# Kernel optimization log

Measured on AMD Instinct MI355X. Metric: run time of the kernel, lower is better.

## Reference

```python
import jax, jax.numpy as jnp
import numpy as np

N, E, CIN, CHID, DIM, KS = 6000, 192000, 32, 64, 3, 5
K = KS ** DIM          # 125 total spline kernel weights
S = 2 ** DIM           # 8 nonzero linear B-spline basis products per edge


def spline_conv(x, edge_index, pseudo, W, root, bias):
    """SplineConv, degree-1 open B-spline, mean aggregation, root weight + bias.
    x: [N, Cin], edge_index: [2, E], pseudo: [E, DIM] in [0,1],
    W: [K, Cin, Cout], root: [Cin, Cout], bias: [Cout].
    """
    src, dst = edge_index[0], edge_index[1]
    cin = x.shape[1]
    # open spline: KS-1 intervals over [0,1]
    u = pseudo * (KS - 1)                               # [E, DIM]
    i0 = jnp.clip(jnp.floor(u), 0, KS - 2).astype(jnp.int32)
    frac = u - i0                                       # [E, DIM]
    bits = (jnp.arange(S)[:, None] >> jnp.arange(DIM)[None, :]) & 1   # [S, DIM]
    strides = KS ** jnp.arange(DIM - 1, -1, -1)         # row-major flattening
    idx = jnp.sum((i0[:, None, :] + bits[None, :, :]) * strides, axis=-1)  # [E, S]
    basis = jnp.prod(jnp.where(bits[None, :, :] == 1,
                               frac[:, None, :], 1.0 - frac[:, None, :]), axis=-1)  # [E, S]
    x_j = x[src]                                        # gather: [E, Cin]
    vals = (basis[..., None] * x_j[:, None, :]).reshape(E * S, cin)
    keys = (dst[:, None] * K + idx).reshape(E * S)
    # bucket basis-weighted source features per (dst node, kernel index)
    T = jax.ops.segment_sum(vals, keys, num_segments=N * K).reshape(N, K, cin)
    out = jnp.einsum('nki,kio->no', T, W)               # [N, Cout]
    deg = jax.ops.segment_sum(jnp.ones((E,), jnp.float32), dst, num_segments=N)
    out = out / jnp.maximum(deg, 1.0)[:, None]          # mean aggregation
    return out + x @ root + bias


def _conv_params(key, cin):
    k1, k2 = jax.random.split(key)
    w_scale = 1.0 / np.sqrt(cin * S)
    W = jax.random.normal(k1, (K, cin, CHID), jnp.float32) * w_scale
    root = jax.random.normal(k2, (cin, CHID), jnp.float32) * (1.0 / np.sqrt(cin))
    b = jnp.zeros((CHID,), jnp.float32)
    return W, root, b


def setup_inputs() -> dict:
    key = jax.random.key(0)
    ks = jax.random.split(key, 10)
    inp = {
        'x': jax.random.normal(ks[0], (N, CIN), jnp.float32),
        'hidden': jax.random.normal(ks[1], (N, CHID), jnp.float32),
        'edge_index': jax.random.randint(ks[2], (2, E), 0, N, dtype=jnp.int32),
        'edge_attr': jax.random.uniform(ks[3], (E, DIM), jnp.float32),
    }
    for i, (name, cin) in enumerate([('xr', CIN), ('hr', CHID), ('xz', CIN),
                                     ('hz', CHID), ('xn', CIN), ('hn', CHID)]):
        W, root, b = _conv_params(ks[4 + i], cin)
        inp[f'W_{name}'] = W
        inp[f'root_{name}'] = root
        inp[f'b_{name}'] = b
    return inp


def reference(x, hidden, edge_index, edge_attr,
              W_xr, root_xr, b_xr, W_hr, root_hr, b_hr,
              W_xz, root_xz, b_xz, W_hz, root_hz, b_hz,
              W_xn, root_xn, b_xn, W_hn, root_hn, b_hn):
    hr_out = spline_conv(hidden, edge_index, edge_attr, W_hr, root_hr, b_hr)
    r = jax.nn.sigmoid(spline_conv(x, edge_index, edge_attr, W_xr, root_xr, b_xr) + hr_out)
    z = jax.nn.sigmoid(spline_conv(x, edge_index, edge_attr, W_xz, root_xz, b_xz)
                       + spline_conv(hidden, edge_index, edge_attr, W_hz, root_hz, b_hz))
    # NOTE: the original torch forward reuses self.hr (not self.hn) here; replicated faithfully.
    n = jnp.tanh(spline_conv(x, edge_index, edge_attr, W_xn, root_xn, b_xn) + r * hr_out)
    h_new = (1.0 - z) * n + z * hidden
    return h_new
```

## Files before the change

### kernel.cpp

```cpp
#include <hip/hip_runtime.h>
#include <math.h>

#define NN_   6000
#define EE_   192000
#define CIN_  32
#define CHID_ 64
#define KK_   125
#define EB_   32
#define CH1_  4
#define CH2_  8
#define CPB_  16

static __device__ __forceinline__ unsigned short f2bf(float f) {
    unsigned int u = __builtin_bit_cast(unsigned int, f);
    u += 0x7fff + ((u >> 16) & 1);
    return (unsigned short)(u >> 16);
}
static __device__ __forceinline__ float bf2f(unsigned short h) {
    unsigned int u = ((unsigned int)h) << 16;
    return __builtin_bit_cast(float, u);
}

#define PK1_ (192 * KK_ * CIN_)
#define PK2_ (128 * KK_ * CHID_)
#define CB_  ((EE_ + 255) / 256)
__global__ __launch_bounds__(256) void count_pack_kernel(
    const int* __restrict__ ei, int* __restrict__ deg,
    const float* __restrict__ W_xr, const float* __restrict__ W_xz,
    const float* __restrict__ W_xn, const float* __restrict__ W_hr,
    const float* __restrict__ W_hz,
    unsigned short* __restrict__ B1t, unsigned short* __restrict__ B2t)
{
    const int b = blockIdx.x;
    if (b < CB_) {
        int e = b * 256 + threadIdx.x;
        if (e < EE_) atomicAdd(&deg[ei[EE_ + e]], 1);
        return;
    }
    int gid = (b - CB_) * 256 + threadIdx.x;
    if (gid < PK1_) {
        int n  = gid / (KK_ * CIN_);
        int kk = gid % (KK_ * CIN_);
        int conv = n >> 6, o = n & 63;
        const float* W = (conv == 0) ? W_xr : ((conv == 1) ? W_xz : W_xn);
        B1t[gid] = f2bf(W[(size_t)kk * 64 + o]);
    } else if (gid < PK1_ + PK2_) {
        int g2 = gid - PK1_;
        int n  = g2 / (KK_ * CHID_);
        int kk = g2 % (KK_ * CHID_);
        int conv = n >> 6, o = n & 63;
        const float* W = (conv == 0) ? W_hr : W_hz;
        B2t[g2] = f2bf(W[(size_t)kk * 64 + o]);
    }
}

__global__ __launch_bounds__(1024) void scan_kernel(
    const int* __restrict__ deg, int* __restrict__ offs, int* __restrict__ cursor)
{
    __shared__ int part[1024];
    const int tid = threadIdx.x;
    const int CH = (NN_ + 1023) / 1024;
    const int base = tid * CH;
    int loc[CH];
    int s = 0;
#pragma unroll
    for (int i = 0; i < CH; ++i) {
        int v = (base + i < NN_) ? deg[base + i] : 0;
        loc[i] = s; s += v;
    }
    part[tid] = s;
    __syncthreads();
    for (int off = 1; off < 1024; off <<= 1) {
        int v = (tid >= off) ? part[tid - off] : 0;
        __syncthreads();
        part[tid] += v;
        __syncthreads();
    }
    const int pre = (tid > 0) ? part[tid - 1] : 0;
#pragma unroll
    for (int i = 0; i < CH; ++i) {
        if (base + i < NN_) {
            offs[base + i]   = pre + loc[i];
            cursor[base + i] = pre + loc[i];
        }
    }
    if (tid == 1023) offs[NN_] = part[1023];
}

__global__ __launch_bounds__(256) void prep_kernel(
    const int* __restrict__ ei, const float* __restrict__ attr,
    int* __restrict__ cursor, float4* __restrict__ meta_s, int* __restrict__ src_s)
{
    int e = blockIdx.x * 256 + threadIdx.x;
    if (e >= EE_) return;
    const int dst = ei[EE_ + e];
    const int p   = atomicAdd(&cursor[dst], 1);
    float f[3]; int i0[3];
#pragma unroll
    for (int d = 0; d < 3; ++d) {
        float u  = attr[e * 3 + d] * 4.0f;
        float fl = floorf(u);
        fl = fminf(fmaxf(fl, 0.0f), 3.0f);
        i0[d] = (int)fl;
        f[d]  = u - fl;
    }
    meta_s[p] = make_float4(f[0], f[1], f[2],
        __int_as_float(i0[0] * 25 + i0[1] * 5 + i0[2]));
    src_s[p] = ei[e];
}

template<int C>
__global__ __launch_bounds__(256) void build_T_kernel(
    const float4* __restrict__ meta_s, const int* __restrict__ src_s,
    const float* __restrict__ feat, const int* __restrict__ offs,
    unsigned short* __restrict__ Tb)
{
    constexpr int PAD   = C + 2;
    constexpr int NPAIR = C / 2;
    constexpr int EPI   = (C == 32) ? 2 : 1;
    constexpr int PPW   = (C == 32) ? 4 : 8;
    __shared__ float        Tl[KK_ * PAD];
    __shared__ int          s_base[EB_];
    __shared__ float        s_basis[EB_ * 8];
    __shared__ int          s_src[EB_];
    __shared__ unsigned int s_fb[EB_ * NPAIR];

    const int node = blockIdx.x;
    const int tid  = threadIdx.x;
    const int wave = tid >> 6;
    const int lane = tid & 63;

    for (int i = tid; i < KK_ * PAD; i += 256) Tl[i] = 0.f;

    const int j0 = offs[node], j1 = offs[node + 1];

    const int e2   = (EPI == 2) ? (lane >> 5) : 0;
    const int s_c  = (EPI == 2) ? ((lane >> 2) & 7) : (lane >> 3);
    const int pl   = (EPI == 2) ? (lane & 3) : (lane & 7);
    const int pidx = wave * PPW + pl;
    const int cb0 = s_c & 1, cb1 = (s_c >> 1) & 1, cb2 = (s_c >> 2) & 1;
    const int offc = cb0 * 25 + cb1 * 5 + cb2;

    __syncthreads();

    for (int jb = j0; jb < j1; jb += EB_) {
        const int m = min(EB_, j1 - jb);

        if (tid < m) {
            const float4 mt = meta_s[jb + tid];
            s_src[tid]  = src_s[jb + tid];
            s_base[tid] = __float_as_int(mt.w);
            const float f0 = mt.x, f1 = mt.y, f2 = mt.z;
            const float g0 = 1.f - f0, g1 = 1.f - f1, g2 = 1.f - f2;
            float4 blo = make_float4(g0 * g1 * g2, f0 * g1 * g2,
                                     g0 * f1 * g2, f0 * f1 * g2);
            float4 bhi = make_float4(g0 * g1 * f2, f0 * g1 * f2,
                                     g0 * f1 * f2, f0 * f1 * f2);
            *(float4*)&s_basis[tid * 8]     = blo;
            *(float4*)&s_basis[tid * 8 + 4] = bhi;
        }
        __syncthreads();

        for (int u = tid; u < m * NPAIR; u += 256) {
            const int r = u / NPAIR, q = u % NPAIR;
            float2 v = *(const float2*)&feat[(size_t)s_src[r] * C + 2 * q];
            s_fb[u] = (unsigned int)f2bf(v.x) | ((unsigned int)f2bf(v.y) << 16);
        }
        __syncthreads();

        for (int eb = 0; eb < m; eb += EPI) {
            const int e = eb + e2;
            if (EPI == 1 || e < m) {
                const int   base = s_base[e];
                const float p    = s_basis[e * 8 + s_c];
                const unsigned int fp = s_fb[e * NPAIR + pidx];
                const float fx = bf2f((unsigned short)(fp & 0xffff));
                const float fy = bf2f((unsigned short)(fp >> 16));
                float* cell = &Tl[(base + offc) * PAD + 2 * pidx];
                cell[0] += p * fx;
                cell[1] += p * fy;
            }
        }
        __syncthreads();
    }

    unsigned int* To = (unsigned int*)(Tb + (size_t)node * (KK_ * C));
    for (int u = tid; u < KK_ * NPAIR; u += 256) {
        int k = u / NPAIR, pp = u % NPAIR;
        unsigned int lo = f2bf(Tl[k * PAD + 2 * pp]);
        unsigned int hi = f2bf(Tl[k * PAD + 2 * pp + 1]);
        To[u] = lo | (hi << 16);
    }
}

template<int NT, int NTF, int CPB>
static __device__ __forceinline__ void gemm_body(
    unsigned char* arena,
    const unsigned short* __restrict__ A, const unsigned short* __restrict__ Bt,
    unsigned short* __restrict__ P, int M, int Kd, int chunk, int zhalf)
{
    constexpr int SPC   = 2;
    constexpr int COLS  = SPC * 32;
    constexpr int BP    = COLS + 8;
    constexpr int NFRAG = NT / 16;
    constexpr int CSP   = NT + 8;
    unsigned short (*Bs)[BP] = (unsigned short(*)[BP])arena;

    using bf16x8 = __attribute__((ext_vector_type(8))) short;
    using f32x4  = __attribute__((ext_vector_type(4))) float;

    const int tid  = threadIdx.x;
    const int wave = tid >> 6;
    const int lane = tid & 63;
    const int quad = lane >> 4;
    const int l16  = lane & 15;
    const int m0   = blockIdx.x * 64;
    const unsigned short* Bp = Bt + (size_t)zhalf * NT * Kd;

    const int  arow   = m0 + wave * 16 + l16;
    const bool avalid = arow < M;
    const unsigned short* Ap = A + (size_t)(avalid ? arow : 0) * Kd;

    f32x4 acc[NFRAG];
#pragma unroll
    for (int f = 0; f < NFRAG; ++f) acc[f] = (f32x4){0.f, 0.f, 0.f, 0.f};

    for (int cc = 0; cc < CPB; ++cc) {
        const int k0 = (chunk * CPB + cc) * COLS;
        if (k0 >= Kd) break;
        const int ksz = min(Kd - k0, COLS);

        __syncthreads();

        constexpr int BUNITS = NT * COLS / 8;
        for (int u = tid; u < BUNITS; u += 256) {
            const int row = u / (COLS / 8);
            const int cq  = (u % (COLS / 8)) * 8;
            uint4 v = make_uint4(0u, 0u, 0u, 0u);
            if (cq < ksz) v = *(const uint4*)(Bp + (size_t)row * Kd + k0 + cq);
            *(uint4*)&Bs[row][cq] = v;
        }

        uint4 afr[SPC];
#pragma unroll
        for (int s = 0; s < SPC; ++s) {
            const int k = k0 + s * 32 + quad * 8;
            afr[s] = (avalid && k < Kd) ? *(const uint4*)(Ap + k)
                                        : make_uint4(0u, 0u, 0u, 0u);
        }

        __syncthreads();

#pragma unroll
        for (int s = 0; s < SPC; ++s) {
            bf16x8 af = __builtin_bit_cast(bf16x8, afr[s]);
#pragma unroll
            for (int f = 0; f < NFRAG; ++f) {
                bf16x8 bfv = *(bf16x8*)&Bs[f * 16 + l16][s * 32 + quad * 8];
                acc[f] = __builtin_amdgcn_mfma_f32_16x16x32_bf16(af, bfv, acc[f], 0, 0, 0);
            }
        }
    }

    __syncthreads();
    unsigned short* Cs = (unsigned short*)arena;
    const int rbase = wave * 16 + quad * 4;
#pragma unroll
    for (int f = 0; f < NFRAG; ++f) {
        const int col = f * 16 + l16;
#pragma unroll
        for (int r = 0; r < 4; ++r)
            Cs[(rbase + r) * CSP + col] = f2bf(acc[f][r]);
    }
    __syncthreads();
    unsigned short* Pc = P + ((size_t)chunk * M + m0) * NTF + zhalf * NT;
    constexpr int UNITS = 64 * NT / 8;
    for (int u = tid; u < UNITS; u += 256) {
        const int row = (u * 8) / NT, col = (u * 8) % NT;
        if (m0 + row < M)
            *(uint4*)&Pc[(size_t)row * NTF + col] = *(const uint4*)&Cs[row * CSP + col];
    }
}

__global__ __launch_bounds__(256) void gemm_all_kernel(
    const unsigned short* __restrict__ Tx, const unsigned short* __restrict__ B1t,
    unsigned short* __restrict__ P1,
    const unsigned short* __restrict__ Th, const unsigned short* __restrict__ B2t,
    unsigned short* __restrict__ P2)
{
    __shared__ __align__(16) unsigned char arena[128 * 72 * 2];
    const int y = blockIdx.y;
    if (y < CH2_) {
        gemm_body<128, 128, CPB_>(arena, Th, B2t, P2, NN_, KK_ * CHID_, y, 0);
    } else {
        const int g = y - CH2_;
        gemm_body<96, 192, CPB_>(arena, Tx, B1t, P1, NN_, KK_ * CIN_, g >> 1, g & 1);
    }
}

__global__ __launch_bounds__(256) void epilogue_kernel(
    const unsigned short* __restrict__ P1, const unsigned short* __restrict__ P2,
    const int* __restrict__ offs,
    const float* __restrict__ x, const float* __restrict__ hidden,
    const float* __restrict__ root_xr, const float* __restrict__ root_hr,
    const float* __restrict__ root_xz, const float* __restrict__ root_hz,
    const float* __restrict__ root_xn,
    const float* __restrict__ b_xr, const float* __restrict__ b_hr,
    const float* __restrict__ b_xz, const float* __restrict__ b_hz,
    const float* __restrict__ b_xn,
    float* __restrict__ out)
{
    __shared__ float xsh[4][32];
    __shared__ float hsh[4][64];
    const int w = threadIdx.x >> 6;
    const int o = threadIdx.x & 63;
    const int m = blockIdx.x * 4 + w;
    if (m >= NN_) return;

    if (o < 32) xsh[w][o] = x[(size_t)m * 32 + o];
    const float hval = hidden[(size_t)m * 64 + o];
    hsh[w][o] = hval;

    float axr = 0.f, axz = 0.f, axn = 0.f;
#pragma unroll
    for (int c = 0; c < CH1_; ++c) {
        const unsigned short* p = P1 + ((size_t)c * NN_ + m) * 192;
        axr += bf2f(p[o]); axz += bf2f(p[64 + o]); axn += bf2f(p[128 + o]);
    }
    float ahr = 0.f, ahz = 0.f;
#pragma unroll
    for (int c = 0; c < CH2_; ++c) {
        const unsigned short* p = P2 + ((size_t)c * NN_ + m) * 128;
        ahr += bf2f(p[o]); ahz += bf2f(p[64 + o]);
    }

    const int   dg   = offs[m + 1] - offs[m];
    const float dinv = 1.0f / fmaxf((float)dg, 1.0f);
    axr *= dinv; axz *= dinv; axn *= dinv; ahr *= dinv; ahz *= dinv;

    float sxr = 0.f, sxz = 0.f, sxn = 0.f;
#pragma unroll
    for (int c = 0; c < CIN_; ++c) {
        float xv = xsh[w][c];
        sxr += xv * root_xr[c * 64 + o];
        sxz += xv * root_xz[c * 64 + o];
        sxn += xv * root_xn[c * 64 + o];
    }
    float shr = 0.f, shz = 0.f;
#pragma unroll
    for (int c = 0; c < CHID_; ++c) {
        float hv = hsh[w][c];
        shr += hv * root_hr[c * 64 + o];
        shz += hv * root_hz[c * 64 + o];
    }

    const float conv_xr = axr + sxr + b_xr[o];
    const float conv_xz = axz + sxz + b_xz[o];
    const float conv_xn = axn + sxn + b_xn[o];
    const float hr_out  = ahr + shr + b_hr[o];
    const float conv_hz = ahz + shz + b_hz[o];

    const float rg = 1.0f / (1.0f + expf(-(conv_xr + hr_out)));
    const float zg = 1.0f / (1.0f + expf(-(conv_xz + conv_hz)));
    const float ng = tanhf(conv_xn + rg * hr_out);
    out[(size_t)m * 64 + o] = (1.0f - zg) * ng + zg * hval;
}

extern "C" void kernel_launch(void* const* d_in, const int* in_sizes, int n_in,
                              void* d_out, int out_size, void* d_ws, size_t ws_size,
                              hipStream_t stream)
{
    const float* x       = (const float*)d_in[0];
    const float* hidden  = (const float*)d_in[1];
    const int*   ei      = (const int*)  d_in[2];
    const float* attr    = (const float*)d_in[3];
    const float* W_xr    = (const float*)d_in[4];
    const float* root_xr = (const float*)d_in[5];
    const float* b_xr    = (const float*)d_in[6];
    const float* W_hr    = (const float*)d_in[7];
    const float* root_hr = (const float*)d_in[8];
    const float* b_hr    = (const float*)d_in[9];
    const float* W_xz    = (const float*)d_in[10];
    const float* root_xz = (const float*)d_in[11];
    const float* b_xz    = (const float*)d_in[12];
    const float* W_hz    = (const float*)d_in[13];
    const float* root_hz = (const float*)d_in[14];
    const float* b_hz    = (const float*)d_in[15];
    const float* W_xn    = (const float*)d_in[16];
    const float* root_xn = (const float*)d_in[17];
    const float* b_xn    = (const float*)d_in[18];
    float* out = (float*)d_out;

    char* w = (char*)d_ws;
    unsigned short* Tx  = (unsigned short*)w; w += (size_t)NN_ * KK_ * CIN_  * 2;
    unsigned short* Th  = (unsigned short*)w; w += (size_t)NN_ * KK_ * CHID_ * 2;
    unsigned short* B1t = (unsigned short*)w; w += (size_t)192 * KK_ * CIN_  * 2;
    unsigned short* B2t = (unsigned short*)w; w += (size_t)128 * KK_ * CHID_ * 2;
    unsigned short* P1  = (unsigned short*)w; w += (size_t)CH1_ * NN_ * 192 * 2;
    unsigned short* P2  = (unsigned short*)w; w += (size_t)CH2_ * NN_ * 128 * 2;
    float4* meta_s = (float4*)w; w += (size_t)EE_ * 16;
    int* src_s  = (int*)w;   w += (size_t)EE_ * 4;
    int* deg    = (int*)w;   w += (size_t)NN_ * 4;
    int* offs   = (int*)w;   w += (size_t)(NN_ + 4) * 4;
    int* cursor = (int*)w;   w += (size_t)NN_ * 4;

    const int MT = (NN_ + 63) / 64;

    hipMemsetAsync(deg, 0, (size_t)NN_ * 4, stream);

    const int PACKB = (PK1_ + PK2_ + 255) / 256;
    count_pack_kernel<<<CB_ + PACKB, 256, 0, stream>>>(
        ei, deg, W_xr, W_xz, W_xn, W_hr, W_hz, B1t, B2t);

    scan_kernel<<<1, 1024, 0, stream>>>(deg, offs, cursor);
    prep_kernel<<<(EE_ + 255) / 256, 256, 0, stream>>>(ei, attr, cursor, meta_s, src_s);

    build_T_kernel<CHID_><<<NN_, 256, 0, stream>>>(meta_s, src_s, hidden, offs, Th);
    build_T_kernel<CIN_><<<NN_, 256, 0, stream>>>(meta_s, src_s, x, offs, Tx);

    gemm_all_kernel<<<dim3(MT, CH2_ + 2 * CH1_), 256, 0, stream>>>(
        Tx, B1t, P1, Th, B2t, P2);

    epilogue_kernel<<<(NN_ + 3) / 4, 256, 0, stream>>>(
        P1, P2, offs, x, hidden,
        root_xr, root_hr, root_xz, root_hz, root_xn,
        b_xr, b_hr, b_xz, b_hz, b_xn, out);
}
```

Measured before the change: 287.0 us.

## Build per-node spline bucket tensor with MFMA instead of LDS scatter-adds

Each block of up to 32 edges is now turned into a dense bf16 basis matrix (128 kernel slots × 32 edges) and a transposed bf16 feature matrix (C × 32 edges) in shared memory. The per-node T bucket is then accumulated in registers with 16x16x32 bf16 MFMA instructions. This replaces the serial per-edge read-modify-write accumulation into an fp32 shared-memory tile. In exchange, the basis weights are rounded to bf16, the 128×40 basis tile must be re-zeroed for every edge block, and the matmul does mostly zero-work because the basis matrix is sparse.

```diff
diff --git a/kernel.cpp b/kernel.cpp
--- a/kernel.cpp
+++ b/kernel.cpp
@@ -115,81 +115,93 @@
     const float* __restrict__ feat, const int* __restrict__ offs,
     unsigned short* __restrict__ Tb)
 {
-    constexpr int PAD   = C + 2;
-    constexpr int NPAIR = C / 2;
-    constexpr int EPI   = (C == 32) ? 2 : 1;
-    constexpr int PPW   = (C == 32) ? 4 : 8;
-    __shared__ float        Tl[KK_ * PAD];
-    __shared__ int          s_base[EB_];
-    __shared__ float        s_basis[EB_ * 8];
-    __shared__ int          s_src[EB_];
-    __shared__ unsigned int s_fb[EB_ * NPAIR];
-
-    const int node = blockIdx.x;
+    constexpr int MP  = 40;
+    constexpr int CT  = C / 16;
+    constexpr int CPT = C / 8;
+    using bf16x8 = __attribute__((ext_vector_type(8))) short;
+    using f32x4  = __attribute__((ext_vector_type(4))) float;
+
+    __shared__ __align__(16) unsigned short Mt [128 * MP];
+    __shared__ __align__(16) unsigned short fbT[C   * MP];
+    __shared__ int s_src[EB_];
+
     const int tid  = threadIdx.x;
     const int wave = tid >> 6;
     const int lane = tid & 63;
-
-    for (int i = tid; i < KK_ * PAD; i += 256) Tl[i] = 0.f;
+    const int quad = lane >> 4;
+    const int l16  = lane & 15;
+    const int node = blockIdx.x;
+
+    for (int i = tid; i < C * MP / 8; i += 256)
+        ((uint4*)fbT)[i] = make_uint4(0u, 0u, 0u, 0u);
 
     const int j0 = offs[node], j1 = offs[node + 1];
 
-    const int e2   = (EPI == 2) ? (lane >> 5) : 0;
-    const int s_c  = (EPI == 2) ? ((lane >> 2) & 7) : (lane >> 3);
-    const int pl   = (EPI == 2) ? (lane & 3) : (lane & 7);
-    const int pidx = wave * PPW + pl;
-    const int cb0 = s_c & 1, cb1 = (s_c >> 1) & 1, cb2 = (s_c >> 2) & 1;
-    const int offc = cb0 * 25 + cb1 * 5 + cb2;
-
-    __syncthreads();
+    f32x4 acc[2][CT];
+#pragma unroll
+    for (int t = 0; t < 2; ++t)
+#pragma unroll
+        for (int ct = 0; ct < CT; ++ct) acc[t][ct] = (f32x4){0.f, 0.f, 0.f, 0.f};
 
     for (int jb = j0; jb < j1; jb += EB_) {
         const int m = min(EB_, j1 - jb);
 
+        __syncthreads();
+        for (int i = tid; i < 128 * MP / 8; i += 256)
+            ((uint4*)Mt)[i] = make_uint4(0u, 0u, 0u, 0u);
+        if (tid < m) s_src[tid] = src_s[jb + tid];
+        __syncthreads();
+
         if (tid < m) {
             const float4 mt = meta_s[jb + tid];
-            s_src[tid]  = src_s[jb + tid];
-            s_base[tid] = __float_as_int(mt.w);
+            const int base = __float_as_int(mt.w);
             const float f0 = mt.x, f1 = mt.y, f2 = mt.z;
             const float g0 = 1.f - f0, g1 = 1.f - f1, g2 = 1.f - f2;
-            float4 blo = make_float4(g0 * g1 * g2, f0 * g1 * g2,
-                                     g0 * f1 * g2, f0 * f1 * g2);
-            float4 bhi = make_float4(g0 * g1 * f2, f0 * g1 * f2,
-                                     g0 * f1 * f2, f0 * f1 * f2);
-            *(float4*)&s_basis[tid * 8]     = blo;
-            *(float4*)&s_basis[tid * 8 + 4] = bhi;
-        }
-        __syncthreads();
-
-        for (int u = tid; u < m * NPAIR; u += 256) {
-            const int r = u / NPAIR, q = u % NPAIR;
-            float2 v = *(const float2*)&feat[(size_t)s_src[r] * C + 2 * q];
-            s_fb[u] = (unsigned int)f2bf(v.x) | ((unsigned int)f2bf(v.y) << 16);
-        }
-        __syncthreads();
-
-        for (int eb = 0; eb < m; eb += EPI) {
-            const int e = eb + e2;
-            if (EPI == 1 || e < m) {
-                const int   base = s_base[e];
-                const float p    = s_basis[e * 8 + s_c];
-                const unsigned int fp = s_fb[e * NPAIR + pidx];
-                const float fx = bf2f((unsigned short)(fp & 0xffff));
-                const float fy = bf2f((unsigned short)(fp >> 16));
-                float* cell = &Tl[(base + offc) * PAD + 2 * pidx];
-                cell[0] += p * fx;
-                cell[1] += p * fy;
+            const float bb[8] = {g0*g1*g2, f0*g1*g2, g0*f1*g2, f0*f1*g2,
+                                 g0*g1*f2, f0*g1*f2, g0*f1*f2, f0*f1*f2};
+            const int oc[8] = {0, 25, 5, 30, 1, 26, 6, 31};
+#pragma unroll
+            for (int s = 0; s < 8; ++s)
+                Mt[(base + oc[s]) * MP + tid] = f2bf(bb[s]);
+        }
+        {
+            const int e = tid >> 3, cg = (tid & 7) * CPT;
+            if (e < m) {
+                const float* fr = &feat[(size_t)s_src[e] * C + cg];
+#pragma unroll
+                for (int c4 = 0; c4 < CPT; c4 += 4) {
+                    float4 v = *(const float4*)(fr + c4);
+                    fbT[(cg + c4 + 0) * MP + e] = f2bf(v.x);
+                    fbT[(cg + c4 + 1) * MP + e] = f2bf(v.y);
+                    fbT[(cg + c4 + 2) * MP + e] = f2bf(v.z);
+                    fbT[(cg + c4 + 3) * MP + e] = f2bf(v.w);
+                }
             }
         }
         __syncthreads();
-    }
-
-    unsigned int* To = (unsigned int*)(Tb + (size_t)node * (KK_ * C));
-    for (int u = tid; u < KK_ * NPAIR; u += 256) {
-        int k = u / NPAIR, pp = u % NPAIR;
-        unsigned int lo = f2bf(Tl[k * PAD + 2 * pp]);
-        unsigned int hi = f2bf(Tl[k * PAD + 2 * pp + 1]);
-        To[u] = lo | (hi << 16);
+
+        bf16x8 a0 = *(const bf16x8*)&Mt[((wave * 2 + 0) * 16 + l16) * MP + quad * 8];
+        bf16x8 a1 = *(const bf16x8*)&Mt[((wave * 2 + 1) * 16 + l16) * MP + quad * 8];
+#pragma unroll
+        for (int ct = 0; ct < CT; ++ct) {
+            bf16x8 b = *(const bf16x8*)&fbT[(ct * 16 + l16) * MP + quad * 8];
+            acc[0][ct] = __builtin_amdgcn_mfma_f32_16x16x32_bf16(a0, b, acc[0][ct], 0, 0, 0);
+            acc[1][ct] = __builtin_amdgcn_mfma_f32_16x16x32_bf16(a1, b, acc[1][ct], 0, 0, 0);
+        }
+    }
+
+    unsigned short* To = Tb + (size_t)node * (KK_ * C);
+#pragma unroll
+    for (int t = 0; t < 2; ++t) {
+        const int rbase = (wave * 2 + t) * 16 + quad * 4;
+#pragma unroll
+        for (int ct = 0; ct < CT; ++ct) {
+#pragma unroll
+            for (int r = 0; r < 4; ++r) {
+                const int R = rbase + r;
+                if (R < KK_) To[R * C + ct * 16 + l16] = f2bf(acc[t][ct][r]);
+            }
+        }
     }
 }
 
```

Result: faster. 251.8 us (-12.2%).
